# Kernel tuning notes

Hardware: AMD Instinct MI355X
Metric: run time of the kernel (lower is better)

Reference implementation:

```python
import jax, jax.numpy as jnp
import numpy as np

DIM = 512
NUM_HEADS = 8
HEAD_DIM = DIM // NUM_HEADS
SCALE = HEAD_DIM ** -0.5


def setup_inputs() -> dict:
    key = jax.random.key(0)
    ks = jax.random.split(key, 6)
    B, N = 2, 4096
    x = jax.random.normal(ks[0], (B, N, DIM), dtype=jnp.float32)
    # xavier_uniform for qkv [3*dim, dim] and proj [dim, dim] (torch Linear weight layout [out,in])
    lim_qkv = float(np.sqrt(6.0 / (3 * DIM + DIM)))
    w_qkv = jax.random.uniform(ks[1], (3 * DIM, DIM), minval=-lim_qkv, maxval=lim_qkv, dtype=jnp.float32)
    lim_p = float(np.sqrt(6.0 / (DIM + DIM)))
    w_proj = jax.random.uniform(ks[2], (DIM, DIM), minval=-lim_p, maxval=lim_p, dtype=jnp.float32)
    b_proj = jnp.zeros((DIM,), dtype=jnp.float32)
    ln_gamma = jnp.ones((DIM,), dtype=jnp.float32)
    ln_beta = jnp.zeros((DIM,), dtype=jnp.float32)
    return {"x": x, "w_qkv": w_qkv, "w_proj": w_proj, "b_proj": b_proj,
            "ln_gamma": ln_gamma, "ln_beta": ln_beta}


def _attention(x, w_qkv, w_proj, b_proj, ln_gamma, ln_beta):
    B, N, C = x.shape
    qkv = jnp.einsum('bnc,dc->bnd', x, w_qkv)              # [B,N,3C]
    qkv = qkv.reshape(B, N, 3, NUM_HEADS, HEAD_DIM)
    qkv = jnp.transpose(qkv, (2, 0, 3, 1, 4))              # [3,B,H,N,Dh]
    q, k, v = qkv[0], qkv[1], qkv[2]
    attn = jnp.einsum('bhnd,bhmd->bhnm', q, k) * SCALE     # [B,H,N,N]
    attn = jax.nn.softmax(attn, axis=-1)
    # dropout is identity in eval mode
    out = jnp.einsum('bhnm,bhmd->bhnd', attn, v)           # [B,H,N,Dh]
    out = jnp.transpose(out, (0, 2, 1, 3)).reshape(B, N, C)
    out = jnp.einsum('bnc,dc->bnd', out, w_proj) + b_proj
    y = x + out
    mean = jnp.mean(y, axis=-1, keepdims=True)
    var = jnp.var(y, axis=-1, keepdims=True)
    return (y - mean) / jnp.sqrt(var + 1e-5) * ln_gamma + ln_beta


def reference(x, w_qkv, w_proj, b_proj, ln_gamma, ln_beta):
    return _attention(x, w_qkv, w_proj, b_proj, ln_gamma, ln_beta)
```

## Files before the change

kernel.cpp:

```cpp
#include <hip/hip_runtime.h>
#include <hip/hip_bf16.h>

#define SEQ    4096
#define CDIM   512
#define NHEADS 8
#define HDIM   64
#define QSCALE 0.18033688f

typedef __attribute__((ext_vector_type(4))) float f32x4;
typedef __attribute__((ext_vector_type(8))) short bf16x8;

__device__ __forceinline__ int swz(int row, int col) {
    int b = (row << 7) + (col << 1);
    b ^= (row & 7) << 4;
    return b >> 1;
}

__device__ __forceinline__ short f2bf(float f) {
    union { __hip_bfloat16 h; short s; } u;
    u.h = __float2bfloat16(f);
    return u.s;
}

__device__ __forceinline__ void gl16(const void* g, void* l) {
    __builtin_amdgcn_global_load_lds(
        (const __attribute__((address_space(1))) unsigned int*)g,
        (__attribute__((address_space(3))) unsigned int*)l,
        16, 0, 0);
}

__global__ __launch_bounds__(256) void cvt3_k(
    const float* __restrict__ a0, short* __restrict__ o0, int c0,
    const float* __restrict__ a1, short* __restrict__ o1, int c1,
    const float* __restrict__ a2, short* __restrict__ o2, int c2)
{
    const int total = c0 + c1 + c2;
    int i = blockIdx.x * 256 + threadIdx.x;
    const int stride = gridDim.x * 256;
    for (; i < total; i += stride) {
        const float* a; short* o; int j;
        if (i < c0)           { a = a0; o = o0; j = i; }
        else if (i < c0 + c1) { a = a1; o = o1; j = i - c0; }
        else                  { a = a2; o = o2; j = i - c0 - c1; }
        float4 v = ((const float4*)a)[j];
        short4 r;
        r.x = f2bf(v.x); r.y = f2bf(v.y); r.z = f2bf(v.z); r.w = f2bf(v.w);
        ((short4*)o)[j] = r;
    }
}

__global__ __launch_bounds__(256) void qkv_gemm_k(
    const short* __restrict__ xb, const short* __restrict__ wb,
    short* __restrict__ qb, short* __restrict__ kb, short* __restrict__ vtb)
{
    __shared__ alignas(16) short As[2][128 * 64];
    __shared__ alignas(16) short Bs[2][128 * 64];
    const int tid  = threadIdx.x;
    const int lane = tid & 63;
    const int l15  = lane & 15;
    const int lg   = lane >> 4;
    const int wv   = tid >> 6;
    const int wy   = wv >> 1, wx = wv & 1;
    const int m0 = blockIdx.x * 128;
    const int n0 = blockIdx.y * 128;

    const f32x4 fzero = {0.f, 0.f, 0.f, 0.f};
    f32x4 acc[4][4];
    #pragma unroll
    for (int i = 0; i < 4; ++i)
        #pragma unroll
        for (int j = 0; j < 4; ++j)
            acc[i][j] = fzero;

    const int row0 = wv * 8 + (lane >> 3);
    const int cb   = ((lane & 7) ^ (lane >> 3)) << 4;
    const char* agp = (const char*)xb + (size_t)(m0 + row0) * 1024 + cb;
    const char* bgp = (const char*)wb + (size_t)(n0 + row0) * 1024 + cb;
    char* al0 = (char*)&As[0][0] + wv * 1024;
    char* al1 = (char*)&As[1][0] + wv * 1024;
    char* bl0 = (char*)&Bs[0][0] + wv * 1024;
    char* bl1 = (char*)&Bs[1][0] + wv * 1024;

    #define QSTAGE(al, bl, kofs) do {                                  \
        _Pragma("unroll")                                              \
        for (int i_ = 0; i_ < 4; ++i_) {                               \
            gl16(agp + (kofs) + i_ * 32768, (al) + i_ * 4096);         \
            gl16(bgp + (kofs) + i_ * 32768, (bl) + i_ * 4096);         \
        } } while (0)

    QSTAGE(al0, bl0, 0);

    int cur = 0;
    for (int k0 = 0; k0 < CDIM; k0 += 64) {
        asm volatile("s_waitcnt vmcnt(0)" ::: "memory");
        __syncthreads();
        if (k0 + 64 < CDIM) {
            if (cur == 0) QSTAGE(al1, bl1, (k0 + 64) * 2);
            else          QSTAGE(al0, bl0, (k0 + 64) * 2);
        }
        const short* Ac = cur ? &As[1][0] : &As[0][0];
        const short* Bc = cur ? &Bs[1][0] : &Bs[0][0];

        #pragma unroll
        for (int ks = 0; ks < 2; ++ks) {
            bf16x8 afr[4], bfr[4];
            #pragma unroll
            for (int i = 0; i < 4; ++i) {
                afr[i] = *(const bf16x8*)(&Ac[swz(wy * 64 + i * 16 + l15, ks * 32 + lg * 8)]);
                bfr[i] = *(const bf16x8*)(&Bc[swz(wx * 64 + i * 16 + l15, ks * 32 + lg * 8)]);
            }
            #pragma unroll
            for (int i = 0; i < 4; ++i)
                #pragma unroll
                for (int j = 0; j < 4; ++j)
                    acc[i][j] = __builtin_amdgcn_mfma_f32_16x16x32_bf16(afr[i], bfr[j], acc[i][j], 0, 0, 0);
        }
        cur ^= 1;
    }
    #undef QSTAGE

    #pragma unroll
    for (int j = 0; j < 4; ++j) {
        const int d = n0 + wx * 64 + j * 16 + l15;
        const int s = d >> 9;
        const int h = (d >> 6) & 7;
        const int e = d & 63;
        #pragma unroll
        for (int i = 0; i < 4; ++i) {
            #pragma unroll
            for (int r = 0; r < 4; ++r) {
                const int m  = m0 + wy * 64 + i * 16 + lg * 4 + r;
                const int bb = m >> 12;
                const int n  = m & (SEQ - 1);
                const int bh = bb * NHEADS + h;
                const float v = acc[i][j][r];
                if (s == 0) {
                    qb[(((size_t)bh * SEQ + n) << 6) + e] = f2bf(v * QSCALE);
                } else if (s == 1) {
                    kb[(((size_t)bh * SEQ + n) << 6) + e] = f2bf(v);
                } else {
                    const int c  = n & 63;
                    const int cp = (c & 0x23) | ((c & 0x0C) << 1) | ((c & 0x10) >> 2);
                    vtb[((size_t)bh << 18) + ((size_t)(n >> 6) << 12) + (e << 6) + cp] = f2bf(v);
                }
            }
        }
    }
}

__global__ __launch_bounds__(512) void attn_k(
    const short* __restrict__ qb, const short* __restrict__ kb, const short* __restrict__ vtb,
    short* __restrict__ ob)
{
    __shared__ alignas(16) char smem[81920];
    const int tid  = threadIdx.x;
    const int lane = tid & 63;
    const int l15  = lane & 15;
    const int lg   = lane >> 4;
    const int wv   = (tid >> 6) & 3;
    const int wg   = tid >> 8;
    const int lin  = blockIdx.x;
    const int bh   = lin & 15;
    const int q0   = (lin >> 4) << 7;
    const int b    = bh >> 3, h = bh & 7;
    const int phase = ((lin >> 8) & 1) << 4;
    const size_t base = (size_t)bh * SEQ * HDIM;

    bf16x8 qf[2][2];
    #pragma unroll
    for (int qi = 0; qi < 2; ++qi) {
        const short* qp = qb + base + (size_t)(q0 + wv * 32 + qi * 16 + l15) * HDIM + lg * 8;
        qf[qi][0] = *(const bf16x8*)(qp);
        qf[qi][1] = *(const bf16x8*)(qp + 32);
    }

    const f32x4 fzero = {0.f, 0.f, 0.f, 0.f};
    f32x4 acc[2][4];
    f32x4 lacc[2];
    #pragma unroll
    for (int qi = 0; qi < 2; ++qi) {
        lacc[qi] = fzero;
        #pragma unroll
        for (int di = 0; di < 4; ++di) acc[qi][di] = fzero;
    }

    bf16x8 ones;
    #pragma unroll
    for (int e = 0; e < 8; ++e) ones[e] = (short)0x3F80;

    const int t0  = wv * 128 + lane;
    const int cbs = ((t0 & 7) ^ ((t0 >> 3) & 7)) << 4;
    const int ghb = wg * 262144;
    const char* kgp = (const char*)(kb + base) + ghb + (((t0 >> 3) << 7) + cbs);
    const char* vgp = (const char*)(vtb + ((size_t)bh << 18)) + ghb + (((t0 >> 3) << 7) + cbs);
    char* const gb = smem + wg * 40960;
    char* K0p = gb +     0 + wv * 2048;  const short* Kr0 = (const short*)(gb);
    char* K1p = gb +  8192 + wv * 2048;  const short* Kr1 = (const short*)(gb + 8192);
    char* V0p = gb + 16384 + wv * 2048;  const short* Vr0 = (const short*)(gb + 16384);
    char* V1p = gb + 24576 + wv * 2048;  const short* Vr1 = (const short*)(gb + 24576);
    char* V2p = gb + 32768 + wv * 2048;  const short* Vr2 = (const short*)(gb + 32768);

    bf16x8 paA[2][2], paB[2][2];

    #define TOFS(T) (((phase + (T)) & 31) * 8192)

    #define STAGE(klp, vlp, BOFS) do {                                     \
        _Pragma("unroll")                                                  \
        for (int i_ = 0; i_ < 2; ++i_) {                                   \
            gl16(kgp + (BOFS) + i_ * 1024, (klp) + i_ * 1024);             \
            gl16(vgp + (BOFS) + i_ * 1024, (vlp) + i_ * 1024);             \
        } } while (0)

    #define MFMA16(a_, b_, c_) __builtin_amdgcn_mfma_f32_16x16x32_bf16(a_, b_, c_, 0, 0, 0)

    #define BODY(TILE, KRD, VPR, KSTP, VSTP, PAP, PAN, DOSTG) do {             \
        asm volatile("s_waitcnt vmcnt(0)" ::: "memory");                       \
        __syncthreads();                                                       \
        if (DOSTG) { STAGE(KSTP, VSTP, TOFS((TILE) + 1)); }                    \
        _Pragma("unroll")                                                      \
        for (int ni = 0; ni < 4; ++ni) {                                       \
            bf16x8 kf0 = *(const bf16x8*)(&(KRD)[swz(ni * 16 + l15, lg * 8)]);      \
            bf16x8 kf1 = *(const bf16x8*)(&(KRD)[swz(ni * 16 + l15, 32 + lg * 8)]); \
            f32x4 s0 = fzero, s1 = fzero;                                      \
            s0 = MFMA16(kf0, qf[0][0], s0);                                    \
            s0 = MFMA16(kf1, qf[0][1], s0);                                    \
            s1 = MFMA16(kf0, qf[1][0], s1);                                    \
            s1 = MFMA16(kf1, qf[1][1], s1);                                    \
            bf16x8 v0 = *(const bf16x8*)(&(VPR)[swz(ni * 16 + l15, lg * 8)]);       \
            bf16x8 v1 = *(const bf16x8*)(&(VPR)[swz(ni * 16 + l15, 32 + lg * 8)]);  \
            acc[0][ni] = MFMA16(PAP[0][0], v0, acc[0][ni]);                    \
            acc[0][ni] = MFMA16(PAP[0][1], v1, acc[0][ni]);                    \
            acc[1][ni] = MFMA16(PAP[1][0], v0, acc[1][ni]);                    \
            acc[1][ni] = MFMA16(PAP[1][1], v1, acc[1][ni]);                    \
            if (ni == 0) { lacc[0] = MFMA16(PAP[0][0], ones, lacc[0]);         \
                           lacc[0] = MFMA16(PAP[0][1], ones, lacc[0]); }       \
            if (ni == 1) { lacc[1] = MFMA16(PAP[1][0], ones, lacc[1]);         \
                           lacc[1] = MFMA16(PAP[1][1], ones, lacc[1]); }       \
            _Pragma("unroll")                                                  \
            for (int r = 0; r < 4; ++r) {                                      \
                PAN[0][ni >> 1][(ni & 1) * 4 + r] = f2bf(__builtin_amdgcn_exp2f(s0[r])); \
                PAN[1][ni >> 1][(ni & 1) * 4 + r] = f2bf(__builtin_amdgcn_exp2f(s1[r])); \
            }                                                                  \
        }                                                                      \
    } while (0)

    STAGE(K0p, V0p, TOFS(0));
    asm volatile("s_waitcnt vmcnt(0)" ::: "memory");
    __syncthreads();
    STAGE(K1p, V1p, TOFS(1));
    #pragma unroll
    for (int ni = 0; ni < 4; ++ni) {
        bf16x8 kf0 = *(const bf16x8*)(&Kr0[swz(ni * 16 + l15, lg * 8)]);
        bf16x8 kf1 = *(const bf16x8*)(&Kr0[swz(ni * 16 + l15, 32 + lg * 8)]);
        f32x4 s0 = fzero, s1 = fzero;
        s0 = MFMA16(kf0, qf[0][0], s0);
        s0 = MFMA16(kf1, qf[0][1], s0);
        s1 = MFMA16(kf0, qf[1][0], s1);
        s1 = MFMA16(kf1, qf[1][1], s1);
        #pragma unroll
        for (int r = 0; r < 4; ++r) {
            paA[0][ni >> 1][(ni & 1) * 4 + r] = f2bf(__builtin_amdgcn_exp2f(s0[r]));
            paA[1][ni >> 1][(ni & 1) * 4 + r] = f2bf(__builtin_amdgcn_exp2f(s1[r]));
        }
    }

    for (int i = 0; i < 5; ++i) {
        BODY(6 * i + 1, Kr1, Vr0, K0p, V2p, paA, paB, 1);
        BODY(6 * i + 2, Kr0, Vr1, K1p, V0p, paB, paA, 1);
        BODY(6 * i + 3, Kr1, Vr2, K0p, V1p, paA, paB, 1);
        BODY(6 * i + 4, Kr0, Vr0, K1p, V2p, paB, paA, 1);
        BODY(6 * i + 5, Kr1, Vr1, K0p, V0p, paA, paB, 1);
        BODY(6 * i + 6, Kr0, Vr2, K1p, V1p, paB, paA, 1);
    }
    BODY(31, Kr1, Vr0, K0p, V2p, paA, paB, 0);

    #pragma unroll
    for (int dd = 0; dd < 4; ++dd) {
        bf16x8 v0 = *(const bf16x8*)(&Vr1[swz(dd * 16 + l15, lg * 8)]);
        bf16x8 v1 = *(const bf16x8*)(&Vr1[swz(dd * 16 + l15, 32 + lg * 8)]);
        acc[0][dd] = MFMA16(paB[0][0], v0, acc[0][dd]);
        acc[0][dd] = MFMA16(paB[0][1], v1, acc[0][dd]);
        acc[1][dd] = MFMA16(paB[1][0], v0, acc[1][dd]);
        acc[1][dd] = MFMA16(paB[1][1], v1, acc[1][dd]);
    }
    lacc[0] = MFMA16(paB[0][0], ones, lacc[0]);
    lacc[0] = MFMA16(paB[0][1], ones, lacc[0]);
    lacc[1] = MFMA16(paB[1][0], ones, lacc[1]);
    lacc[1] = MFMA16(paB[1][1], ones, lacc[1]);
    #undef BODY
    #undef MFMA16
    #undef STAGE
    #undef TOFS

    __syncthreads();
    float* xch = (float*)smem;
    const int xi = (wv * 64 + lane) * 44;
    if (wg == 1) {
        #pragma unroll
        for (int qi = 0; qi < 2; ++qi) {
            #pragma unroll
            for (int di = 0; di < 4; ++di)
                *(f32x4*)(xch + xi + qi * 16 + di * 4) = acc[qi][di];
            *(f32x4*)(xch + xi + 32 + qi * 4) = lacc[qi];
        }
    }
    __syncthreads();
    if (wg == 0) {
        #pragma unroll
        for (int qi = 0; qi < 2; ++qi) {
            #pragma unroll
            for (int di = 0; di < 4; ++di)
                acc[qi][di] += *(const f32x4*)(xch + xi + qi * 16 + di * 4);
            lacc[qi] += *(const f32x4*)(xch + xi + 32 + qi * 4);
        }
        #pragma unroll
        for (int qi = 0; qi < 2; ++qi) {
            float inv[4];
            #pragma unroll
            for (int r = 0; r < 4; ++r) inv[r] = 1.0f / lacc[qi][r];
            #pragma unroll
            for (int di = 0; di < 4; ++di) {
                const int e = di * 16 + l15;
                #pragma unroll
                for (int r = 0; r < 4; ++r) {
                    const int qn = q0 + wv * 32 + qi * 16 + lg * 4 + r;
                    ob[((size_t)(b * SEQ + qn) << 9) + h * 64 + e] = f2bf(acc[qi][di][r] * inv[r]);
                }
            }
        }
    }
}

__global__ __launch_bounds__(256) void proj_k(
    const short* __restrict__ ao, const short* __restrict__ wpb,
    const float* __restrict__ bp, const float* __restrict__ x,
    float* __restrict__ y)
{
    __shared__ alignas(16) short As[2][128 * 64];
    __shared__ alignas(16) short Bs[2][128 * 64];
    const int tid  = threadIdx.x;
    const int lane = tid & 63;
    const int l15  = lane & 15;
    const int lg   = lane >> 4;
    const int wv   = tid >> 6;
    const int wy   = wv >> 1, wx = wv & 1;
    const int m0 = blockIdx.x * 128;
    const int n0 = blockIdx.y * 128;

    const f32x4 fzero = {0.f, 0.f, 0.f, 0.f};
    f32x4 acc[4][4];
    #pragma unroll
    for (int i = 0; i < 4; ++i)
        #pragma unroll
        for (int j = 0; j < 4; ++j)
            acc[i][j] = fzero;

    const int row0 = wv * 8 + (lane >> 3);
    const int cb   = ((lane & 7) ^ (lane >> 3)) << 4;
    const char* agp = (const char*)ao  + (size_t)(m0 + row0) * 1024 + cb;
    const char* bgp = (const char*)wpb + (size_t)(n0 + row0) * 1024 + cb;
    char* al0 = (char*)&As[0][0] + wv * 1024;
    char* al1 = (char*)&As[1][0] + wv * 1024;
    char* bl0 = (char*)&Bs[0][0] + wv * 1024;
    char* bl1 = (char*)&Bs[1][0] + wv * 1024;

    #define PSTAGE(al, bl, kofs) do {                                  \
        _Pragma("unroll")                                              \
        for (int i_ = 0; i_ < 4; ++i_) {                               \
            gl16(agp + (kofs) + i_ * 32768, (al) + i_ * 4096);         \
            gl16(bgp + (kofs) + i_ * 32768, (bl) + i_ * 4096);         \
        } } while (0)

    PSTAGE(al0, bl0, 0);

    int cur = 0;
    for (int k0 = 0; k0 < CDIM; k0 += 64) {
        asm volatile("s_waitcnt vmcnt(0)" ::: "memory");
        __syncthreads();
        if (k0 + 64 < CDIM) {
            if (cur == 0) PSTAGE(al1, bl1, (k0 + 64) * 2);
            else          PSTAGE(al0, bl0, (k0 + 64) * 2);
        }
        const short* Ac = cur ? &As[1][0] : &As[0][0];
        const short* Bc = cur ? &Bs[1][0] : &Bs[0][0];

        #pragma unroll
        for (int ks = 0; ks < 2; ++ks) {
            bf16x8 afr[4], bfr[4];
            #pragma unroll
            for (int i = 0; i < 4; ++i) {
                afr[i] = *(const bf16x8*)(&Ac[swz(wy * 64 + i * 16 + l15, ks * 32 + lg * 8)]);
                bfr[i] = *(const bf16x8*)(&Bc[swz(wx * 64 + i * 16 + l15, ks * 32 + lg * 8)]);
            }
            #pragma unroll
            for (int i = 0; i < 4; ++i)
                #pragma unroll
                for (int j = 0; j < 4; ++j)
                    acc[i][j] = __builtin_amdgcn_mfma_f32_16x16x32_bf16(afr[i], bfr[j], acc[i][j], 0, 0, 0);
        }
        cur ^= 1;
    }
    #undef PSTAGE

    #pragma unroll
    for (int i = 0; i < 4; ++i) {
        #pragma unroll
        for (int j = 0; j < 4; ++j) {
            const int d = n0 + wx * 64 + j * 16 + l15;
            #pragma unroll
            for (int r = 0; r < 4; ++r) {
                const int m = m0 + wy * 64 + i * 16 + lg * 4 + r;
                const size_t idx = (size_t)m * CDIM + d;
                y[idx] = acc[i][j][r] + bp[d] + x[idx];
            }
        }
    }
}

__global__ __launch_bounds__(256) void ln_k(
    float* __restrict__ y, const float* __restrict__ gm, const float* __restrict__ bt)
{
    const int lane = threadIdx.x & 63;
    const int row  = blockIdx.x * 4 + (threadIdx.x >> 6);
    float* p = y + (size_t)row * CDIM;
    float4 a = *(const float4*)(p + lane * 4);
    float4 b = *(const float4*)(p + 256 + lane * 4);
    float s = a.x + a.y + a.z + a.w + b.x + b.y + b.z + b.w;
    float q = a.x * a.x + a.y * a.y + a.z * a.z + a.w * a.w
            + b.x * b.x + b.y * b.y + b.z * b.z + b.w * b.w;
    #pragma unroll
    for (int mm = 1; mm < 64; mm <<= 1) {
        s += __shfl_xor(s, mm, 64);
        q += __shfl_xor(q, mm, 64);
    }
    const float mean = s * (1.0f / CDIM);
    const float var  = q * (1.0f / CDIM) - mean * mean;
    const float inv  = rsqrtf(var + 1e-5f);
    float4 g0 = *(const float4*)(gm + lane * 4);
    float4 g1 = *(const float4*)(gm + 256 + lane * 4);
    float4 t0 = *(const float4*)(bt + lane * 4);
    float4 t1 = *(const float4*)(bt + 256 + lane * 4);
    float4 r0, r1;
    r0.x = (a.x - mean) * inv * g0.x + t0.x;
    r0.y = (a.y - mean) * inv * g0.y + t0.y;
    r0.z = (a.z - mean) * inv * g0.z + t0.z;
    r0.w = (a.w - mean) * inv * g0.w + t0.w;
    r1.x = (b.x - mean) * inv * g1.x + t1.x;
    r1.y = (b.y - mean) * inv * g1.y + t1.y;
    r1.z = (b.z - mean) * inv * g1.z + t1.z;
    r1.w = (b.w - mean) * inv * g1.w + t1.w;
    *(float4*)(p + lane * 4) = r0;
    *(float4*)(p + 256 + lane * 4) = r1;
}

extern "C" void kernel_launch(void* const* d_in, const int* in_sizes, int n_in,
                              void* d_out, int out_size, void* d_ws, size_t ws_size,
                              hipStream_t stream)
{
    const float* x      = (const float*)d_in[0];
    const float* w_qkv  = (const float*)d_in[1];
    const float* w_proj = (const float*)d_in[2];
    const float* b_proj = (const float*)d_in[3];
    const float* gamma  = (const float*)d_in[4];
    const float* beta   = (const float*)d_in[5];
    float* out = (float*)d_out;

    const size_t qkv_elems = (size_t)16 * SEQ * HDIM;
    short* qb    = (short*)d_ws;
    short* kb    = qb + qkv_elems;
    short* vtb   = kb + qkv_elems;
    short* ob    = vtb + qkv_elems;
    short* xb    = ob;
    short* wqkvb = ob + qkv_elems;
    short* wpb   = wqkvb + (size_t)3 * CDIM * CDIM;

    cvt3_k    <<<dim3(1024),   256, 0, stream>>>(
        x, xb, (2 * SEQ * CDIM) / 4,
        w_qkv, wqkvb, (3 * CDIM * CDIM) / 4,
        w_proj, wpb, (CDIM * CDIM) / 4);
    qkv_gemm_k<<<dim3(64, 12), 256, 0, stream>>>(xb, wqkvb, qb, kb, vtb);
    attn_k    <<<dim3(512),    512, 0, stream>>>(qb, kb, vtb, ob);
    proj_k    <<<dim3(64, 4),  256, 0, stream>>>(ob, wpb, b_proj, x, out);
    ln_k      <<<dim3(2048),   256, 0, stream>>>(out, gamma, beta);
}
```

Baseline: 117.5 us.

## Switch attention inner loop to 32x32x16 MFMA and compute row sums on VALU

Rewrites the attention kernel's QK^T and PV products to use 32x32x16 bf16 MFMA tiles instead of 16x16x32. The V layout permutation in the QKV kernel changes to match the new operand fragment order. Softmax row sums are now accumulated as scalar adds and combined with a cross-lane shuffle, replacing the extra MFMAs against a ones vector. The phase offset that staggered tile start positions across blocks is dropped, which removes a spread of memory accesses across blocks.

```diff
diff --git a/kernel.cpp b/kernel.cpp
--- a/kernel.cpp
+++ b/kernel.cpp
@@ -7,8 +7,9 @@
 #define HDIM   64
 #define QSCALE 0.18033688f
 
-typedef __attribute__((ext_vector_type(4))) float f32x4;
-typedef __attribute__((ext_vector_type(8))) short bf16x8;
+typedef __attribute__((ext_vector_type(4)))  float f32x4;
+typedef __attribute__((ext_vector_type(16))) float f32x16;
+typedef __attribute__((ext_vector_type(8)))  short bf16x8;
 
 __device__ __forceinline__ int swz(int row, int col) {
     int b = (row << 7) + (col << 1);
@@ -140,7 +141,7 @@
                     kb[(((size_t)bh * SEQ + n) << 6) + e] = f2bf(v);
                 } else {
                     const int c  = n & 63;
-                    const int cp = (c & 0x23) | ((c & 0x0C) << 1) | ((c & 0x10) >> 2);
+                    const int cp = (c & 0x33) | ((c & 0x04) << 1) | ((c & 0x08) >> 1);
                     vtb[((size_t)bh << 18) + ((size_t)(n >> 6) << 12) + (e << 6) + cp] = f2bf(v);
                 }
             }
@@ -155,38 +156,29 @@
     __shared__ alignas(16) char smem[81920];
     const int tid  = threadIdx.x;
     const int lane = tid & 63;
-    const int l15  = lane & 15;
-    const int lg   = lane >> 4;
+    const int l31  = lane & 31;
+    const int h8   = (lane >> 5) << 3;
     const int wv   = (tid >> 6) & 3;
     const int wg   = tid >> 8;
     const int lin  = blockIdx.x;
     const int bh   = lin & 15;
     const int q0   = (lin >> 4) << 7;
     const int b    = bh >> 3, h = bh & 7;
-    const int phase = ((lin >> 8) & 1) << 4;
     const size_t base = (size_t)bh * SEQ * HDIM;
 
-    bf16x8 qf[2][2];
-    #pragma unroll
-    for (int qi = 0; qi < 2; ++qi) {
-        const short* qp = qb + base + (size_t)(q0 + wv * 32 + qi * 16 + l15) * HDIM + lg * 8;
-        qf[qi][0] = *(const bf16x8*)(qp);
-        qf[qi][1] = *(const bf16x8*)(qp + 32);
-    }
-
-    const f32x4 fzero = {0.f, 0.f, 0.f, 0.f};
-    f32x4 acc[2][4];
-    f32x4 lacc[2];
-    #pragma unroll
-    for (int qi = 0; qi < 2; ++qi) {
-        lacc[qi] = fzero;
-        #pragma unroll
-        for (int di = 0; di < 4; ++di) acc[qi][di] = fzero;
-    }
-
-    bf16x8 ones;
-    #pragma unroll
-    for (int e = 0; e < 8; ++e) ones[e] = (short)0x3F80;
+    bf16x8 qf0, qf1, qf2, qf3;
+    {
+        const short* qp = qb + base + (size_t)(q0 + wv * 32 + l31) * HDIM + h8;
+        qf0 = *(const bf16x8*)(qp);
+        qf1 = *(const bf16x8*)(qp + 16);
+        qf2 = *(const bf16x8*)(qp + 32);
+        qf3 = *(const bf16x8*)(qp + 48);
+    }
+
+    f32x16 accA, accB;
+    #pragma unroll
+    for (int z = 0; z < 16; ++z) { accA[z] = 0.f; accB[z] = 0.f; }
+    float lsum = 0.f;
 
     const int t0  = wv * 128 + lane;
     const int cbs = ((t0 & 7) ^ ((t0 >> 3) & 7)) << 4;
@@ -200,67 +192,83 @@
     char* V1p = gb + 24576 + wv * 2048;  const short* Vr1 = (const short*)(gb + 24576);
     char* V2p = gb + 32768 + wv * 2048;  const short* Vr2 = (const short*)(gb + 32768);
 
-    bf16x8 paA[2][2], paB[2][2];
-
-    #define TOFS(T) (((phase + (T)) & 31) * 8192)
-
-    #define STAGE(klp, vlp, BOFS) do {                                     \
+    bf16x8 paA[4], paB[4];
+
+    #define STAGE(klp, vlp, TI) do {                                       \
         _Pragma("unroll")                                                  \
         for (int i_ = 0; i_ < 2; ++i_) {                                   \
-            gl16(kgp + (BOFS) + i_ * 1024, (klp) + i_ * 1024);             \
-            gl16(vgp + (BOFS) + i_ * 1024, (vlp) + i_ * 1024);             \
+            gl16(kgp + (TI) * 8192 + i_ * 1024, (klp) + i_ * 1024);        \
+            gl16(vgp + (TI) * 8192 + i_ * 1024, (vlp) + i_ * 1024);        \
         } } while (0)
 
-    #define MFMA16(a_, b_, c_) __builtin_amdgcn_mfma_f32_16x16x32_bf16(a_, b_, c_, 0, 0, 0)
-
-    #define BODY(TILE, KRD, VPR, KSTP, VSTP, PAP, PAN, DOSTG) do {             \
-        asm volatile("s_waitcnt vmcnt(0)" ::: "memory");                       \
-        __syncthreads();                                                       \
-        if (DOSTG) { STAGE(KSTP, VSTP, TOFS((TILE) + 1)); }                    \
-        _Pragma("unroll")                                                      \
-        for (int ni = 0; ni < 4; ++ni) {                                       \
-            bf16x8 kf0 = *(const bf16x8*)(&(KRD)[swz(ni * 16 + l15, lg * 8)]);      \
-            bf16x8 kf1 = *(const bf16x8*)(&(KRD)[swz(ni * 16 + l15, 32 + lg * 8)]); \
-            f32x4 s0 = fzero, s1 = fzero;                                      \
-            s0 = MFMA16(kf0, qf[0][0], s0);                                    \
-            s0 = MFMA16(kf1, qf[0][1], s0);                                    \
-            s1 = MFMA16(kf0, qf[1][0], s1);                                    \
-            s1 = MFMA16(kf1, qf[1][1], s1);                                    \
-            bf16x8 v0 = *(const bf16x8*)(&(VPR)[swz(ni * 16 + l15, lg * 8)]);       \
-            bf16x8 v1 = *(const bf16x8*)(&(VPR)[swz(ni * 16 + l15, 32 + lg * 8)]);  \
-            acc[0][ni] = MFMA16(PAP[0][0], v0, acc[0][ni]);                    \
-            acc[0][ni] = MFMA16(PAP[0][1], v1, acc[0][ni]);                    \
-            acc[1][ni] = MFMA16(PAP[1][0], v0, acc[1][ni]);                    \
-            acc[1][ni] = MFMA16(PAP[1][1], v1, acc[1][ni]);                    \
-            if (ni == 0) { lacc[0] = MFMA16(PAP[0][0], ones, lacc[0]);         \
-                           lacc[0] = MFMA16(PAP[0][1], ones, lacc[0]); }       \
-            if (ni == 1) { lacc[1] = MFMA16(PAP[1][0], ones, lacc[1]);         \
-                           lacc[1] = MFMA16(PAP[1][1], ones, lacc[1]); }       \
-            _Pragma("unroll")                                                  \
-            for (int r = 0; r < 4; ++r) {                                      \
-                PAN[0][ni >> 1][(ni & 1) * 4 + r] = f2bf(__builtin_amdgcn_exp2f(s0[r])); \
-                PAN[1][ni >> 1][(ni & 1) * 4 + r] = f2bf(__builtin_amdgcn_exp2f(s1[r])); \
-            }                                                                  \
-        }                                                                      \
+    #define MFMA32(a_, b_, c_) __builtin_amdgcn_mfma_f32_32x32x16_bf16(a_, b_, c_, 0, 0, 0)
+
+    #define QKPV(KRD, VPR, B2, ACC, PAP, PAN) do {                              \
+        f32x16 s_;                                                              \
+        _Pragma("unroll")                                                       \
+        for (int z_ = 0; z_ < 16; ++z_) s_[z_] = 0.f;                           \
+        {                                                                       \
+            bf16x8 k0_ = *(const bf16x8*)(&(KRD)[swz((B2) * 32 + l31,  0 + h8)]); \
+            bf16x8 k1_ = *(const bf16x8*)(&(KRD)[swz((B2) * 32 + l31, 16 + h8)]); \
+            bf16x8 k2_ = *(const bf16x8*)(&(KRD)[swz((B2) * 32 + l31, 32 + h8)]); \
+            bf16x8 k3_ = *(const bf16x8*)(&(KRD)[swz((B2) * 32 + l31, 48 + h8)]); \
+            s_ = MFMA32(k0_, qf0, s_);                                          \
+            s_ = MFMA32(k1_, qf1, s_);                                          \
+            s_ = MFMA32(k2_, qf2, s_);                                          \
+            s_ = MFMA32(k3_, qf3, s_);                                          \
+        }                                                                       \
+        {                                                                       \
+            bf16x8 v0_ = *(const bf16x8*)(&(VPR)[swz((B2) * 32 + l31,  0 + h8)]); \
+            bf16x8 v1_ = *(const bf16x8*)(&(VPR)[swz((B2) * 32 + l31, 16 + h8)]); \
+            bf16x8 v2_ = *(const bf16x8*)(&(VPR)[swz((B2) * 32 + l31, 32 + h8)]); \
+            bf16x8 v3_ = *(const bf16x8*)(&(VPR)[swz((B2) * 32 + l31, 48 + h8)]); \
+            ACC = MFMA32((PAP)[0], v0_, ACC);                                   \
+            ACC = MFMA32((PAP)[1], v1_, ACC);                                   \
+            ACC = MFMA32((PAP)[2], v2_, ACC);                                   \
+            ACC = MFMA32((PAP)[3], v3_, ACC);                                   \
+        }                                                                       \
+        _Pragma("unroll")                                                       \
+        for (int e_ = 0; e_ < 8; ++e_) {                                        \
+            float p0_ = __builtin_amdgcn_exp2f(s_[e_]);                         \
+            float p1_ = __builtin_amdgcn_exp2f(s_[8 + e_]);                     \
+            lsum += p0_ + p1_;                                                  \
+            (PAN)[(B2) * 2][e_]     = f2bf(p0_);                                \
+            (PAN)[(B2) * 2 + 1][e_] = f2bf(p1_);                                \
+        }                                                                       \
     } while (0)
 
-    STAGE(K0p, V0p, TOFS(0));
+    #define BODY(TILE, KRD, VPR, KSTP, VSTP, PAP, PAN, DOSTG) do {         \
+        asm volatile("s_waitcnt vmcnt(0)" ::: "memory");                   \
+        __syncthreads();                                                   \
+        if (DOSTG) { STAGE(KSTP, VSTP, (TILE) + 1); }                      \
+        QKPV(KRD, VPR, 0, accA, PAP, PAN);                                 \
+        QKPV(KRD, VPR, 1, accB, PAP, PAN);                                 \
+    } while (0)
+
+    STAGE(K0p, V0p, 0);
     asm volatile("s_waitcnt vmcnt(0)" ::: "memory");
     __syncthreads();
-    STAGE(K1p, V1p, TOFS(1));
-    #pragma unroll
-    for (int ni = 0; ni < 4; ++ni) {
-        bf16x8 kf0 = *(const bf16x8*)(&Kr0[swz(ni * 16 + l15, lg * 8)]);
-        bf16x8 kf1 = *(const bf16x8*)(&Kr0[swz(ni * 16 + l15, 32 + lg * 8)]);
-        f32x4 s0 = fzero, s1 = fzero;
-        s0 = MFMA16(kf0, qf[0][0], s0);
-        s0 = MFMA16(kf1, qf[0][1], s0);
-        s1 = MFMA16(kf0, qf[1][0], s1);
-        s1 = MFMA16(kf1, qf[1][1], s1);
-        #pragma unroll
-        for (int r = 0; r < 4; ++r) {
-            paA[0][ni >> 1][(ni & 1) * 4 + r] = f2bf(__builtin_amdgcn_exp2f(s0[r]));
-            paA[1][ni >> 1][(ni & 1) * 4 + r] = f2bf(__builtin_amdgcn_exp2f(s1[r]));
+    STAGE(K1p, V1p, 1);
+    #pragma unroll
+    for (int B2 = 0; B2 < 2; ++B2) {
+        f32x16 s;
+        #pragma unroll
+        for (int z = 0; z < 16; ++z) s[z] = 0.f;
+        bf16x8 k0 = *(const bf16x8*)(&Kr0[swz(B2 * 32 + l31,  0 + h8)]);
+        bf16x8 k1 = *(const bf16x8*)(&Kr0[swz(B2 * 32 + l31, 16 + h8)]);
+        bf16x8 k2 = *(const bf16x8*)(&Kr0[swz(B2 * 32 + l31, 32 + h8)]);
+        bf16x8 k3 = *(const bf16x8*)(&Kr0[swz(B2 * 32 + l31, 48 + h8)]);
+        s = MFMA32(k0, qf0, s);
+        s = MFMA32(k1, qf1, s);
+        s = MFMA32(k2, qf2, s);
+        s = MFMA32(k3, qf3, s);
+        #pragma unroll
+        for (int e = 0; e < 8; ++e) {
+            float p0 = __builtin_amdgcn_exp2f(s[e]);
+            float p1 = __builtin_amdgcn_exp2f(s[8 + e]);
+            lsum += p0 + p1;
+            paA[B2 * 2][e]     = f2bf(p0);
+            paA[B2 * 2 + 1][e] = f2bf(p1);
         }
     }
 
@@ -274,59 +282,65 @@
     }
     BODY(31, Kr1, Vr0, K0p, V2p, paA, paB, 0);
 
-    #pragma unroll
-    for (int dd = 0; dd < 4; ++dd) {
-        bf16x8 v0 = *(const bf16x8*)(&Vr1[swz(dd * 16 + l15, lg * 8)]);
-        bf16x8 v1 = *(const bf16x8*)(&Vr1[swz(dd * 16 + l15, 32 + lg * 8)]);
-        acc[0][dd] = MFMA16(paB[0][0], v0, acc[0][dd]);
-        acc[0][dd] = MFMA16(paB[0][1], v1, acc[0][dd]);
-        acc[1][dd] = MFMA16(paB[1][0], v0, acc[1][dd]);
-        acc[1][dd] = MFMA16(paB[1][1], v1, acc[1][dd]);
-    }
-    lacc[0] = MFMA16(paB[0][0], ones, lacc[0]);
-    lacc[0] = MFMA16(paB[0][1], ones, lacc[0]);
-    lacc[1] = MFMA16(paB[1][0], ones, lacc[1]);
-    lacc[1] = MFMA16(paB[1][1], ones, lacc[1]);
+    {
+        bf16x8 v0 = *(const bf16x8*)(&Vr1[swz(l31,  0 + h8)]);
+        bf16x8 v1 = *(const bf16x8*)(&Vr1[swz(l31, 16 + h8)]);
+        bf16x8 v2 = *(const bf16x8*)(&Vr1[swz(l31, 32 + h8)]);
+        bf16x8 v3 = *(const bf16x8*)(&Vr1[swz(l31, 48 + h8)]);
+        accA = MFMA32(paB[0], v0, accA);
+        accA = MFMA32(paB[1], v1, accA);
+        accA = MFMA32(paB[2], v2, accA);
+        accA = MFMA32(paB[3], v3, accA);
+        bf16x8 w0 = *(const bf16x8*)(&Vr1[swz(32 + l31,  0 + h8)]);
+        bf16x8 w1 = *(const bf16x8*)(&Vr1[swz(32 + l31, 16 + h8)]);
+        bf16x8 w2 = *(const bf16x8*)(&Vr1[swz(32 + l31, 32 + h8)]);
+        bf16x8 w3 = *(const bf16x8*)(&Vr1[swz(32 + l31, 48 + h8)]);
+        accB = MFMA32(paB[0], w0, accB);
+        accB = MFMA32(paB[1], w1, accB);
+        accB = MFMA32(paB[2], w2, accB);
+        accB = MFMA32(paB[3], w3, accB);
+    }
     #undef BODY
-    #undef MFMA16
+    #undef QKPV
+    #undef MFMA32
     #undef STAGE
-    #undef TOFS
 
     __syncthreads();
     float* xch = (float*)smem;
-    const int xi = (wv * 64 + lane) * 44;
+    const int xi = (wv * 64 + lane) * 36;
     if (wg == 1) {
         #pragma unroll
-        for (int qi = 0; qi < 2; ++qi) {
-            #pragma unroll
-            for (int di = 0; di < 4; ++di)
-                *(f32x4*)(xch + xi + qi * 16 + di * 4) = acc[qi][di];
-            *(f32x4*)(xch + xi + 32 + qi * 4) = lacc[qi];
-        }
+        for (int di = 0; di < 4; ++di) {
+            f32x4 ta = { accA[di * 4], accA[di * 4 + 1], accA[di * 4 + 2], accA[di * 4 + 3] };
+            f32x4 tb = { accB[di * 4], accB[di * 4 + 1], accB[di * 4 + 2], accB[di * 4 + 3] };
+            *(f32x4*)(xch + xi + di * 4)      = ta;
+            *(f32x4*)(xch + xi + 16 + di * 4) = tb;
+        }
+        xch[xi + 32] = lsum;
     }
     __syncthreads();
     if (wg == 0) {
         #pragma unroll
-        for (int qi = 0; qi < 2; ++qi) {
-            #pragma unroll
-            for (int di = 0; di < 4; ++di)
-                acc[qi][di] += *(const f32x4*)(xch + xi + qi * 16 + di * 4);
-            lacc[qi] += *(const f32x4*)(xch + xi + 32 + qi * 4);
-        }
-        #pragma unroll
-        for (int qi = 0; qi < 2; ++qi) {
-            float inv[4];
-            #pragma unroll
-            for (int r = 0; r < 4; ++r) inv[r] = 1.0f / lacc[qi][r];
-            #pragma unroll
-            for (int di = 0; di < 4; ++di) {
-                const int e = di * 16 + l15;
-                #pragma unroll
-                for (int r = 0; r < 4; ++r) {
-                    const int qn = q0 + wv * 32 + qi * 16 + lg * 4 + r;
-                    ob[((size_t)(b * SEQ + qn) << 9) + h * 64 + e] = f2bf(acc[qi][di][r] * inv[r]);
-                }
+        for (int di = 0; di < 4; ++di) {
+            f32x4 ta = *(const f32x4*)(xch + xi + di * 4);
+            f32x4 tb = *(const f32x4*)(xch + xi + 16 + di * 4);
+            #pragma unroll
+            for (int r = 0; r < 4; ++r) {
+                accA[di * 4 + r] += ta[r];
+                accB[di * 4 + r] += tb[r];
             }
+        }
+        lsum += xch[xi + 32];
+        const float ltot = lsum + __shfl_xor(lsum, 32, 64);
+        const float linv = 1.0f / ltot;
+        #pragma unroll
+        for (int r = 0; r < 16; ++r) {
+            const int qrow = (r & 3) + 8 * (r >> 2) + ((lane >> 5) << 2);
+            const float il = __shfl(linv, qrow, 64);
+            const int qn = q0 + wv * 32 + qrow;
+            const size_t off = ((size_t)(b * SEQ + qn) << 9) + h * 64 + l31;
+            ob[off]      = f2bf(accA[r] * il);
+            ob[off + 32] = f2bf(accB[r] * il);
         }
     }
 }
```

After: 121.6 us. 1.03x slower.

## Restructure attention KV pipeline into 32-key tiles with 4-deep prefetch ring

Applied to the files above, without the earlier changes.

Changes the attention kernel's K/V streaming from 64-key tiles with a two-buffer, software-pipelined softmax (P from the previous tile) to 32-key tiles held in a four-slot ring buffer with three tiles in flight. The wait before each step is relaxed to vmcnt(4) rather than a full drain, and P is now computed and consumed in the same step. The V-transpose layout written by the QKV kernel is changed to 32-key blocks to match, the phase-offset tile rotation is removed, and LDS use drops. The aim is to hide global load latency behind deeper prefetch, at the cost of twice as many barriers and no overlap of exp with the PV MFMAs across tiles.

```diff
diff --git a/kernel.cpp b/kernel.cpp
--- a/kernel.cpp
+++ b/kernel.cpp
@@ -139,9 +139,9 @@
                 } else if (s == 1) {
                     kb[(((size_t)bh * SEQ + n) << 6) + e] = f2bf(v);
                 } else {
-                    const int c  = n & 63;
-                    const int cp = (c & 0x23) | ((c & 0x0C) << 1) | ((c & 0x10) >> 2);
-                    vtb[((size_t)bh << 18) + ((size_t)(n >> 6) << 12) + (e << 6) + cp] = f2bf(v);
+                    const int c  = n & 31;
+                    const int cp = (c & 3) | ((c & 0x0C) << 1) | ((c & 0x10) >> 2);
+                    vtb[((size_t)bh << 18) + ((size_t)(n >> 5) << 11) + (e << 5) + cp] = f2bf(v);
                 }
             }
         }
@@ -152,7 +152,7 @@
     const short* __restrict__ qb, const short* __restrict__ kb, const short* __restrict__ vtb,
     short* __restrict__ ob)
 {
-    __shared__ alignas(16) char smem[81920];
+    __shared__ alignas(16) char smem[65536];
     const int tid  = threadIdx.x;
     const int lane = tid & 63;
     const int l15  = lane & 15;
@@ -163,7 +163,6 @@
     const int bh   = lin & 15;
     const int q0   = (lin >> 4) << 7;
     const int b    = bh >> 3, h = bh & 7;
-    const int phase = ((lin >> 8) & 1) << 4;
     const size_t base = (size_t)bh * SEQ * HDIM;
 
     bf16x8 qf[2][2];
@@ -188,109 +187,95 @@
     #pragma unroll
     for (int e = 0; e < 8; ++e) ones[e] = (short)0x3F80;
 
-    const int t0  = wv * 128 + lane;
+    const int t0  = wv * 64 + lane;
     const int cbs = ((t0 & 7) ^ ((t0 >> 3) & 7)) << 4;
     const int ghb = wg * 262144;
     const char* kgp = (const char*)(kb + base) + ghb + (((t0 >> 3) << 7) + cbs);
     const char* vgp = (const char*)(vtb + ((size_t)bh << 18)) + ghb + (((t0 >> 3) << 7) + cbs);
-    char* const gb = smem + wg * 40960;
-    char* K0p = gb +     0 + wv * 2048;  const short* Kr0 = (const short*)(gb);
-    char* K1p = gb +  8192 + wv * 2048;  const short* Kr1 = (const short*)(gb + 8192);
-    char* V0p = gb + 16384 + wv * 2048;  const short* Vr0 = (const short*)(gb + 16384);
-    char* V1p = gb + 24576 + wv * 2048;  const short* Vr1 = (const short*)(gb + 24576);
-    char* V2p = gb + 32768 + wv * 2048;  const short* Vr2 = (const short*)(gb + 32768);
-
-    bf16x8 paA[2][2], paB[2][2];
-
-    #define TOFS(T) (((phase + (T)) & 31) * 8192)
-
-    #define STAGE(klp, vlp, BOFS) do {                                     \
-        _Pragma("unroll")                                                  \
-        for (int i_ = 0; i_ < 2; ++i_) {                                   \
-            gl16(kgp + (BOFS) + i_ * 1024, (klp) + i_ * 1024);             \
-            gl16(vgp + (BOFS) + i_ * 1024, (vlp) + i_ * 1024);             \
-        } } while (0)
+    char* const gb = smem + wg * 32768;
+    const short* Kb0 = (const short*)(gb);
+    const short* Kb1 = (const short*)(gb + 4096);
+    const short* Kb2 = (const short*)(gb + 8192);
+    const short* Kb3 = (const short*)(gb + 12288);
+    const short* Vb0 = (const short*)(gb + 16384);
+    const short* Vb1 = (const short*)(gb + 20480);
+    const short* Vb2 = (const short*)(gb + 24576);
+    const short* Vb3 = (const short*)(gb + 28672);
+    char* Ks0 = gb +     0 + wv * 1024;
+    char* Ks1 = gb +  4096 + wv * 1024;
+    char* Ks2 = gb +  8192 + wv * 1024;
+    char* Ks3 = gb + 12288 + wv * 1024;
+    char* Vs0 = gb + 16384 + wv * 1024;
+    char* Vs1 = gb + 20480 + wv * 1024;
+    char* Vs2 = gb + 24576 + wv * 1024;
+    char* Vs3 = gb + 28672 + wv * 1024;
 
     #define MFMA16(a_, b_, c_) __builtin_amdgcn_mfma_f32_16x16x32_bf16(a_, b_, c_, 0, 0, 0)
 
-    #define BODY(TILE, KRD, VPR, KSTP, VSTP, PAP, PAN, DOSTG) do {             \
-        asm volatile("s_waitcnt vmcnt(0)" ::: "memory");                       \
-        __syncthreads();                                                       \
-        if (DOSTG) { STAGE(KSTP, VSTP, TOFS((TILE) + 1)); }                    \
+    #define STAGE2(T_, KS, VS) do {                    \
+        gl16(kgp + (T_) * 4096, (KS));                 \
+        gl16(vgp + (T_) * 4096, (VS));                 \
+    } while (0)
+
+    #define COMPUTE(KR, VR) do {                                               \
+        f32x4 s00 = fzero, s01 = fzero, s10 = fzero, s11 = fzero;              \
+        {                                                                      \
+            bf16x8 kf_;                                                        \
+            kf_ = *(const bf16x8*)(&(KR)[swz(l15, lg * 8)]);                   \
+            s00 = MFMA16(kf_, qf[0][0], s00);                                  \
+            s10 = MFMA16(kf_, qf[1][0], s10);                                  \
+            kf_ = *(const bf16x8*)(&(KR)[swz(l15, 32 + lg * 8)]);              \
+            s00 = MFMA16(kf_, qf[0][1], s00);                                  \
+            s10 = MFMA16(kf_, qf[1][1], s10);                                  \
+            kf_ = *(const bf16x8*)(&(KR)[swz(16 + l15, lg * 8)]);              \
+            s01 = MFMA16(kf_, qf[0][0], s01);                                  \
+            s11 = MFMA16(kf_, qf[1][0], s11);                                  \
+            kf_ = *(const bf16x8*)(&(KR)[swz(16 + l15, 32 + lg * 8)]);         \
+            s01 = MFMA16(kf_, qf[0][1], s01);                                  \
+            s11 = MFMA16(kf_, qf[1][1], s11);                                  \
+        }                                                                      \
+        bf16x8 pa0, pa1;                                                       \
         _Pragma("unroll")                                                      \
-        for (int ni = 0; ni < 4; ++ni) {                                       \
-            bf16x8 kf0 = *(const bf16x8*)(&(KRD)[swz(ni * 16 + l15, lg * 8)]);      \
-            bf16x8 kf1 = *(const bf16x8*)(&(KRD)[swz(ni * 16 + l15, 32 + lg * 8)]); \
-            f32x4 s0 = fzero, s1 = fzero;                                      \
-            s0 = MFMA16(kf0, qf[0][0], s0);                                    \
-            s0 = MFMA16(kf1, qf[0][1], s0);                                    \
-            s1 = MFMA16(kf0, qf[1][0], s1);                                    \
-            s1 = MFMA16(kf1, qf[1][1], s1);                                    \
-            bf16x8 v0 = *(const bf16x8*)(&(VPR)[swz(ni * 16 + l15, lg * 8)]);       \
-            bf16x8 v1 = *(const bf16x8*)(&(VPR)[swz(ni * 16 + l15, 32 + lg * 8)]);  \
-            acc[0][ni] = MFMA16(PAP[0][0], v0, acc[0][ni]);                    \
-            acc[0][ni] = MFMA16(PAP[0][1], v1, acc[0][ni]);                    \
-            acc[1][ni] = MFMA16(PAP[1][0], v0, acc[1][ni]);                    \
-            acc[1][ni] = MFMA16(PAP[1][1], v1, acc[1][ni]);                    \
-            if (ni == 0) { lacc[0] = MFMA16(PAP[0][0], ones, lacc[0]);         \
-                           lacc[0] = MFMA16(PAP[0][1], ones, lacc[0]); }       \
-            if (ni == 1) { lacc[1] = MFMA16(PAP[1][0], ones, lacc[1]);         \
-                           lacc[1] = MFMA16(PAP[1][1], ones, lacc[1]); }       \
-            _Pragma("unroll")                                                  \
-            for (int r = 0; r < 4; ++r) {                                      \
-                PAN[0][ni >> 1][(ni & 1) * 4 + r] = f2bf(__builtin_amdgcn_exp2f(s0[r])); \
-                PAN[1][ni >> 1][(ni & 1) * 4 + r] = f2bf(__builtin_amdgcn_exp2f(s1[r])); \
-            }                                                                  \
+        for (int r_ = 0; r_ < 4; ++r_) {                                       \
+            pa0[r_]     = f2bf(__builtin_amdgcn_exp2f(s00[r_]));               \
+            pa0[4 + r_] = f2bf(__builtin_amdgcn_exp2f(s01[r_]));               \
+            pa1[r_]     = f2bf(__builtin_amdgcn_exp2f(s10[r_]));               \
+            pa1[4 + r_] = f2bf(__builtin_amdgcn_exp2f(s11[r_]));               \
+        }                                                                      \
+        lacc[0] = MFMA16(pa0, ones, lacc[0]);                                  \
+        lacc[1] = MFMA16(pa1, ones, lacc[1]);                                  \
+        _Pragma("unroll")                                                      \
+        for (int di_ = 0; di_ < 4; ++di_) {                                    \
+            bf16x8 vf_ = *(const bf16x8*)(&(VR)[swz(di_ * 8 + (l15 >> 1),      \
+                                                    (l15 & 1) * 32 + lg * 8)]);\
+            acc[0][di_] = MFMA16(pa0, vf_, acc[0][di_]);                       \
+            acc[1][di_] = MFMA16(pa1, vf_, acc[1][di_]);                       \
         }                                                                      \
     } while (0)
 
-    STAGE(K0p, V0p, TOFS(0));
-    asm volatile("s_waitcnt vmcnt(0)" ::: "memory");
-    __syncthreads();
-    STAGE(K1p, V1p, TOFS(1));
-    #pragma unroll
-    for (int ni = 0; ni < 4; ++ni) {
-        bf16x8 kf0 = *(const bf16x8*)(&Kr0[swz(ni * 16 + l15, lg * 8)]);
-        bf16x8 kf1 = *(const bf16x8*)(&Kr0[swz(ni * 16 + l15, 32 + lg * 8)]);
-        f32x4 s0 = fzero, s1 = fzero;
-        s0 = MFMA16(kf0, qf[0][0], s0);
-        s0 = MFMA16(kf1, qf[0][1], s0);
-        s1 = MFMA16(kf0, qf[1][0], s1);
-        s1 = MFMA16(kf1, qf[1][1], s1);
-        #pragma unroll
-        for (int r = 0; r < 4; ++r) {
-            paA[0][ni >> 1][(ni & 1) * 4 + r] = f2bf(__builtin_amdgcn_exp2f(s0[r]));
-            paA[1][ni >> 1][(ni & 1) * 4 + r] = f2bf(__builtin_amdgcn_exp2f(s1[r]));
-        }
-    }
-
-    for (int i = 0; i < 5; ++i) {
-        BODY(6 * i + 1, Kr1, Vr0, K0p, V2p, paA, paB, 1);
-        BODY(6 * i + 2, Kr0, Vr1, K1p, V0p, paB, paA, 1);
-        BODY(6 * i + 3, Kr1, Vr2, K0p, V1p, paA, paB, 1);
-        BODY(6 * i + 4, Kr0, Vr0, K1p, V2p, paB, paA, 1);
-        BODY(6 * i + 5, Kr1, Vr1, K0p, V0p, paA, paB, 1);
-        BODY(6 * i + 6, Kr0, Vr2, K1p, V1p, paB, paA, 1);
-    }
-    BODY(31, Kr1, Vr0, K0p, V2p, paA, paB, 0);
-
-    #pragma unroll
-    for (int dd = 0; dd < 4; ++dd) {
-        bf16x8 v0 = *(const bf16x8*)(&Vr1[swz(dd * 16 + l15, lg * 8)]);
-        bf16x8 v1 = *(const bf16x8*)(&Vr1[swz(dd * 16 + l15, 32 + lg * 8)]);
-        acc[0][dd] = MFMA16(paB[0][0], v0, acc[0][dd]);
-        acc[0][dd] = MFMA16(paB[0][1], v1, acc[0][dd]);
-        acc[1][dd] = MFMA16(paB[1][0], v0, acc[1][dd]);
-        acc[1][dd] = MFMA16(paB[1][1], v1, acc[1][dd]);
-    }
-    lacc[0] = MFMA16(paB[0][0], ones, lacc[0]);
-    lacc[0] = MFMA16(paB[0][1], ones, lacc[0]);
-    lacc[1] = MFMA16(paB[1][0], ones, lacc[1]);
-    lacc[1] = MFMA16(paB[1][1], ones, lacc[1]);
-    #undef BODY
+    #define STEP(T_, KR, VR, KS, VS) do {                          \
+        asm volatile("s_waitcnt vmcnt(4)" ::: "memory");           \
+        __builtin_amdgcn_s_barrier();                              \
+        asm volatile("" ::: "memory");                             \
+        if ((T_) < 61) { STAGE2((T_) + 3, KS, VS); }               \
+        COMPUTE(KR, VR);                                           \
+    } while (0)
+
+    STAGE2(0, Ks0, Vs0);
+    STAGE2(1, Ks1, Vs1);
+    STAGE2(2, Ks2, Vs2);
+
+    for (int it = 0; it < 16; ++it) {
+        const int t = it << 2;
+        STEP(t + 0, Kb0, Vb0, Ks3, Vs3);
+        STEP(t + 1, Kb1, Vb1, Ks0, Vs0);
+        STEP(t + 2, Kb2, Vb2, Ks1, Vs1);
+        STEP(t + 3, Kb3, Vb3, Ks2, Vs2);
+    }
+    #undef STEP
+    #undef COMPUTE
+    #undef STAGE2
     #undef MFMA16
-    #undef STAGE
-    #undef TOFS
 
     __syncthreads();
     float* xch = (float*)smem;
```

Result: faster. 112.4 us (-4.4%).
